# Kernel tuning notes

Hardware: AMD Instinct MI355X
Metric: run time of the kernel (lower is better)

The kernel has to match this reference:

```python
import jax, jax.numpy as jnp
import numpy as np

# module hyperparams (from init_kwargs)
C, O, G, E, W, KS = 64, 64, 16, 128, 7, 2
AH, AS = 2, 2              # activate_height, activate_stride
D = C // G                 # kernel depth per group = 4
N = O // G                 # filters per group = 4
EPS = 1e-5                 # BatchNorm eps
LEAKY = 0.01               # LeakyReLU negative slope
B, T = 2, 512


def setup_inputs() -> dict:
    key = jax.random.key(0)
    k1, k2 = jax.random.split(key)
    x = jax.random.normal(k1, (B, C, E, T), dtype=jnp.float32)
    weight = jax.random.normal(k2, (O, D, E, W), dtype=jnp.float32) * 0.05
    gamma = jnp.ones((O,), jnp.float32)
    beta = jnp.zeros((O,), jnp.float32)
    return {"x": x, "weight": weight, "gamma": gamma, "beta": beta}


def reference(x, weight, gamma, beta):
    b, c, f, T_in = x.shape
    pad = W // 2
    xp = jnp.pad(x, ((0, 0), (0, 0), (0, 0), (pad, pad)))
    t = (T_in + 2 * pad - W) // KS + 1
    # unfold: window index grid [t, W]
    idx = KS * jnp.arange(t)[:, None] + jnp.arange(W)[None, :]
    xu = xp[..., idx]                        # [b, c, f, t, W]
    xu = xu.reshape(b, G, D, f, t, W)        # channel = (g d), group-major
    wg = weight.reshape(G, N, D, f, W)       # out = (g n)
    # broadcast elementwise mul -> [b, g, n, d, f, t, w]
    y = xu[:, :, None] * wg[None, :, :, :, :, None, :]
    y = y.reshape(b, O, D, f, t, W)          # (g n) -> o
    # BatchNorm3d over channel O, training-mode batch stats (biased var)
    mean = y.mean(axis=(0, 2, 3, 4, 5), keepdims=True)
    var = y.var(axis=(0, 2, 3, 4, 5), keepdims=True)
    y = (y - mean) * jax.lax.rsqrt(var + EPS)
    bshape = (1, O, 1, 1, 1, 1)
    y = y * gamma.reshape(bshape) + beta.reshape(bshape)
    ys = y.sum(axis=(2, 5))                  # [b, o, f, t]
    yp = jax.lax.reduce_window(ys, jnp.float32(0), jax.lax.add,
                               (1, 1, AH, 1), (1, 1, AS, 1), 'VALID')  # [b,o,fo,t]
    return jnp.where(yp >= 0, yp, LEAKY * yp)
```

## Files before the change

### kernel.cpp

```cpp
#include <hip/hip_runtime.h>

constexpr int Cc = 64, Oc = 64, Gc = 16, Ec = 128, Wc = 7;
constexpr int Dc = 4, Nc = 4, Bc = 2, Tc = 512, TTc = 256, FOc = 64;
constexpr float EPSf = 1e-5f, LEAKYf = 0.01f;
constexpr float Minv = 1.0f / 1835008.0f;


__global__ __launch_bounds__(256) void stats_k(const float* __restrict__ x,
                                               const float* __restrict__ wgt,
                                               float* __restrict__ acc) {
  int bid = blockIdx.x;
  int fo  = bid & 63;
  int g   = (bid >> 6) & 15;
  int b   = bid >> 10;
  int tid = threadIdx.x;
  int d    = tid >> 6;
  int lane = tid & 63;

  __shared__ float part[4][4][2];

  float m_tot = 0.f, v_tot = 0.f;
#pragma unroll
  for (int f2 = 0; f2 < 2; ++f2) {
    int f = 2 * fo + f2;
    const float4* row4 =
        (const float4*)(x + ((size_t)((b * Cc + g * Dc + d) * Ec + f)) * Tc);
    float4 v0 = row4[lane];
    float4 v1 = row4[lane + 64];
    float se  = v0.x + v0.z + v1.x + v1.z;
    float so  = v0.y + v0.w + v1.y + v1.w;
    float se2 = v0.x * v0.x + v0.z * v0.z + v1.x * v1.x + v1.z * v1.z;
    float so2 = v0.y * v0.y + v0.w * v0.w + v1.y * v1.y + v1.w * v1.w;
#pragma unroll
    for (int off = 1; off < 64; off <<= 1) {
      se  += __shfl_xor(se, off);
      so  += __shfl_xor(so, off);
      se2 += __shfl_xor(se2, off);
      so2 += __shfl_xor(so2, off);
    }
    float x0   = __shfl(v0.x, 0);
    float x1   = __shfl(v0.y, 0);
    float x509 = __shfl(v1.y, 63);
    float x510 = __shfl(v1.z, 63);
    float x511 = __shfl(v1.w, 63);
    if (lane < 4) {
      float ws0 = so - x509 - x511, ws1 = se - x510, ws2 = so - x511;
      float ws3 = se, ws4 = so, ws5 = se - x0, ws6 = so - x1;
      float q0 = so2 - x509 * x509 - x511 * x511, q1 = se2 - x510 * x510;
      float q2 = so2 - x511 * x511, q3 = se2, q4 = so2;
      float q5 = se2 - x0 * x0, q6 = so2 - x1 * x1;
      int o = g * Nc + lane;
      const float* wp = wgt + ((size_t)((o * Dc + d) * Ec + f)) * Wc;
      float w0 = wp[0], w1 = wp[1], w2 = wp[2], w3 = wp[3], w4 = wp[4],
            w5 = wp[5], w6 = wp[6];
      m_tot += ws0 * w0 + ws1 * w1 + ws2 * w2 + ws3 * w3 + ws4 * w4 +
               ws5 * w5 + ws6 * w6;
      v_tot += q0 * w0 * w0 + q1 * w1 * w1 + q2 * w2 * w2 + q3 * w3 * w3 +
               q4 * w4 * w4 + q5 * w5 * w5 + q6 * w6 * w6;
    }
  }
  if (lane < 4) {
    part[d][lane][0] = m_tot;
    part[d][lane][1] = v_tot;
  }
  __syncthreads();
  if (tid < 8) {
    int n = tid >> 1, which = tid & 1;
    float tot = part[0][n][which] + part[1][n][which] + part[2][n][which] +
                part[3][n][which];
    int o = g * Nc + n;
    int slot = bid & 7;
    atomicAdd(&acc[(slot * 2 + which) * 64 + o], tot);
  }
}

__global__ __launch_bounds__(256) void conv_k(const float* __restrict__ x,
                                              const float* __restrict__ wgt,
                                              const float* __restrict__ gamma,
                                              const float* __restrict__ beta,
                                              const float* __restrict__ acc,
                                              float* __restrict__ out) {
  int bid = blockIdx.x;
  int fo  = bid & 63;
  int g   = (bid >> 6) & 15;
  int b   = bid >> 10;
  int tid = threadIdx.x;

  __shared__ float xs[8 * 520];
  __shared__ float wsm[224];
  __shared__ float sA[4], sC[4];

  {
    int f2 = tid >> 7;
    int j  = tid & 127;
#pragma unroll
    for (int dd = 0; dd < 4; ++dd) {
      const float4* src = (const float4*)(
          x + ((size_t)((b * Cc + g * Dc + dd) * Ec + 2 * fo + f2)) * Tc);
      float4 v  = src[j];
      float* row = &xs[(dd * 2 + f2) * 520];
      int q0 = 4 + 4 * j;
      row[((q0 + 0) & 7) * 65 + ((q0 + 0) >> 3)] = v.x;
      row[((q0 + 1) & 7) * 65 + ((q0 + 1) >> 3)] = v.y;
      row[((q0 + 2) & 7) * 65 + ((q0 + 2) >> 3)] = v.z;
      row[((q0 + 3) & 7) * 65 + ((q0 + 3) >> 3)] = v.w;
    }
  }
  if (tid < 64) {
    int r = tid >> 3, jj = tid & 7;
    int q = (jj < 4) ? jj : (512 + jj);
    xs[r * 520 + (q & 7) * 65 + (q >> 3)] = 0.f;
  }
  if (tid < 224) {
    int n = tid / 56, rr = tid % 56;
    int dd = rr / 14, r2 = rr % 14;
    int f2 = r2 / 7, w = r2 % 7;
    int o = g * Nc + n;
    wsm[tid] = wgt[((size_t)((o * Dc + dd) * Ec + 2 * fo + f2)) * Wc + w];
  } else if (tid < 228) {
    int n = tid - 224;
    int o = g * Nc + n;
    float msum = 0.f, esum = 0.f;
#pragma unroll
    for (int s = 0; s < 8; ++s) {
      msum += acc[(s * 2 + 0) * 64 + o];
      esum += acc[(s * 2 + 1) * 64 + o];
    }
    float mean = msum * Minv;
    float e2   = esum * Minv;
    float var  = e2 - mean * mean;
    float a    = gamma[o] * rsqrtf(var + EPSf);
    sA[n] = a;
    sC[n] = 56.0f * (beta[o] - a * mean);
  }
  __syncthreads();

  int n = tid >> 6;
  int j = tid & 63;
  float a0 = 0.f, a1 = 0.f, a2 = 0.f, a3 = 0.f;
#pragma unroll
  for (int r = 0; r < 8; ++r) {
    const float* row = &xs[r * 520];
    float xv[13];
#pragma unroll
    for (int i = 0; i < 13; ++i) {
      int c = 1 + i;
      xv[i] = row[(c & 7) * 65 + (c >> 3) + j];
    }
    const float* wp = &wsm[(n * 8 + r) * 7];
#pragma unroll
    for (int w = 0; w < 7; ++w) {
      float wt = wp[w];
      a0 += xv[w]     * wt;
      a1 += xv[w + 2] * wt;
      a2 += xv[w + 4] * wt;
      a3 += xv[w + 6] * wt;
    }
  }
  float sa = sA[n], sc = sC[n];
  float4 res;
  float r0 = sa * a0 + sc; res.x = (r0 >= 0.f) ? r0 : LEAKYf * r0;
  float r1 = sa * a1 + sc; res.y = (r1 >= 0.f) ? r1 : LEAKYf * r1;
  float r2 = sa * a2 + sc; res.z = (r2 >= 0.f) ? r2 : LEAKYf * r2;
  float r3 = sa * a3 + sc; res.w = (r3 >= 0.f) ? r3 : LEAKYf * r3;
  int o = g * Nc + n;
  float* op = out + ((size_t)((b * Oc + o) * FOc + fo)) * TTc + 4 * j;
  *(float4*)op = res;
}

extern "C" void kernel_launch(void* const* d_in, const int* in_sizes, int n_in,
                              void* d_out, int out_size, void* d_ws, size_t ws_size,
                              hipStream_t stream) {
  (void)in_sizes; (void)n_in; (void)out_size; (void)ws_size;
  const float* x     = (const float*)d_in[0];
  const float* w     = (const float*)d_in[1];
  const float* gamma = (const float*)d_in[2];
  const float* beta  = (const float*)d_in[3];
  float* acc = (float*)d_ws;
  hipMemsetAsync(acc, 0, 1024 * sizeof(float), stream);
  stats_k<<<dim3(Bc * Gc * FOc), dim3(256), 0, stream>>>(x, w, acc);
  conv_k<<<dim3(Bc * Gc * FOc), dim3(256), 0, stream>>>(x, w, gamma, beta, acc,
                                                        (float*)d_out);
}
```

Before: 91.71 us.

## Fuse stats into conv kernel, write raw sums, apply BN+LeakyReLU in finish pass

Replaces the separate stats kernel and the memset with a single fused pass. That pass reads x once, computes the raw windowed conv sums and writes them to workspace. It also produces per-block mean partials from the conv output and variance partials from shared-memory row sums of squares, which removes atomics. A second kernel reduces the partials per channel and applies the affine normalization and LeakyReLU to the raw buffer. The trade is one read of x in place of two, at the cost of an extra write and read of the full output-sized intermediate (about 8 MB).

```diff
diff --git a/kernel.cpp b/kernel.cpp
--- a/kernel.cpp
+++ b/kernel.cpp
@@ -6,80 +6,10 @@
 constexpr float Minv = 1.0f / 1835008.0f;
 
 
-__global__ __launch_bounds__(256) void stats_k(const float* __restrict__ x,
+__global__ __launch_bounds__(256) void fused_k(const float* __restrict__ x,
                                                const float* __restrict__ wgt,
-                                               float* __restrict__ acc) {
-  int bid = blockIdx.x;
-  int fo  = bid & 63;
-  int g   = (bid >> 6) & 15;
-  int b   = bid >> 10;
-  int tid = threadIdx.x;
-  int d    = tid >> 6;
-  int lane = tid & 63;
-
-  __shared__ float part[4][4][2];
-
-  float m_tot = 0.f, v_tot = 0.f;
-#pragma unroll
-  for (int f2 = 0; f2 < 2; ++f2) {
-    int f = 2 * fo + f2;
-    const float4* row4 =
-        (const float4*)(x + ((size_t)((b * Cc + g * Dc + d) * Ec + f)) * Tc);
-    float4 v0 = row4[lane];
-    float4 v1 = row4[lane + 64];
-    float se  = v0.x + v0.z + v1.x + v1.z;
-    float so  = v0.y + v0.w + v1.y + v1.w;
-    float se2 = v0.x * v0.x + v0.z * v0.z + v1.x * v1.x + v1.z * v1.z;
-    float so2 = v0.y * v0.y + v0.w * v0.w + v1.y * v1.y + v1.w * v1.w;
-#pragma unroll
-    for (int off = 1; off < 64; off <<= 1) {
-      se  += __shfl_xor(se, off);
-      so  += __shfl_xor(so, off);
-      se2 += __shfl_xor(se2, off);
-      so2 += __shfl_xor(so2, off);
-    }
-    float x0   = __shfl(v0.x, 0);
-    float x1   = __shfl(v0.y, 0);
-    float x509 = __shfl(v1.y, 63);
-    float x510 = __shfl(v1.z, 63);
-    float x511 = __shfl(v1.w, 63);
-    if (lane < 4) {
-      float ws0 = so - x509 - x511, ws1 = se - x510, ws2 = so - x511;
-      float ws3 = se, ws4 = so, ws5 = se - x0, ws6 = so - x1;
-      float q0 = so2 - x509 * x509 - x511 * x511, q1 = se2 - x510 * x510;
-      float q2 = so2 - x511 * x511, q3 = se2, q4 = so2;
-      float q5 = se2 - x0 * x0, q6 = so2 - x1 * x1;
-      int o = g * Nc + lane;
-      const float* wp = wgt + ((size_t)((o * Dc + d) * Ec + f)) * Wc;
-      float w0 = wp[0], w1 = wp[1], w2 = wp[2], w3 = wp[3], w4 = wp[4],
-            w5 = wp[5], w6 = wp[6];
-      m_tot += ws0 * w0 + ws1 * w1 + ws2 * w2 + ws3 * w3 + ws4 * w4 +
-               ws5 * w5 + ws6 * w6;
-      v_tot += q0 * w0 * w0 + q1 * w1 * w1 + q2 * w2 * w2 + q3 * w3 * w3 +
-               q4 * w4 * w4 + q5 * w5 * w5 + q6 * w6 * w6;
-    }
-  }
-  if (lane < 4) {
-    part[d][lane][0] = m_tot;
-    part[d][lane][1] = v_tot;
-  }
-  __syncthreads();
-  if (tid < 8) {
-    int n = tid >> 1, which = tid & 1;
-    float tot = part[0][n][which] + part[1][n][which] + part[2][n][which] +
-                part[3][n][which];
-    int o = g * Nc + n;
-    int slot = bid & 7;
-    atomicAdd(&acc[(slot * 2 + which) * 64 + o], tot);
-  }
-}
-
-__global__ __launch_bounds__(256) void conv_k(const float* __restrict__ x,
-                                              const float* __restrict__ wgt,
-                                              const float* __restrict__ gamma,
-                                              const float* __restrict__ beta,
-                                              const float* __restrict__ acc,
-                                              float* __restrict__ out) {
+                                               float* __restrict__ raw,
+                                               float* __restrict__ partials) {
   int bid = blockIdx.x;
   int fo  = bid & 63;
   int g   = (bid >> 6) & 15;
@@ -88,23 +18,25 @@
 
   __shared__ float xs[8 * 520];
   __shared__ float wsm[224];
-  __shared__ float sA[4], sC[4];
+  __shared__ float rowsum[4][4][2];
+  __shared__ float QL[8][7];
 
-  {
-    int f2 = tid >> 7;
-    int j  = tid & 127;
+  int f2 = tid >> 7;
+  int j  = tid & 127;
+  float se2p[4], so2p[4];
 #pragma unroll
-    for (int dd = 0; dd < 4; ++dd) {
-      const float4* src = (const float4*)(
-          x + ((size_t)((b * Cc + g * Dc + dd) * Ec + 2 * fo + f2)) * Tc);
-      float4 v  = src[j];
-      float* row = &xs[(dd * 2 + f2) * 520];
-      int q0 = 4 + 4 * j;
-      row[((q0 + 0) & 7) * 65 + ((q0 + 0) >> 3)] = v.x;
-      row[((q0 + 1) & 7) * 65 + ((q0 + 1) >> 3)] = v.y;
-      row[((q0 + 2) & 7) * 65 + ((q0 + 2) >> 3)] = v.z;
-      row[((q0 + 3) & 7) * 65 + ((q0 + 3) >> 3)] = v.w;
-    }
+  for (int dd = 0; dd < 4; ++dd) {
+    const float4* src = (const float4*)(
+        x + ((size_t)((b * Cc + g * Dc + dd) * Ec + 2 * fo + f2)) * Tc);
+    float4 v = src[j];
+    float* row = &xs[(dd * 2 + f2) * 520];
+    int q0 = 4 + 4 * j;
+    row[((q0 + 0) & 7) * 65 + ((q0 + 0) >> 3)] = v.x;
+    row[((q0 + 1) & 7) * 65 + ((q0 + 1) >> 3)] = v.y;
+    row[((q0 + 2) & 7) * 65 + ((q0 + 2) >> 3)] = v.z;
+    row[((q0 + 3) & 7) * 65 + ((q0 + 3) >> 3)] = v.w;
+    se2p[dd] = v.x * v.x + v.z * v.z;
+    so2p[dd] = v.y * v.y + v.w * v.w;
   }
   if (tid < 64) {
     int r = tid >> 3, jj = tid & 7;
@@ -114,29 +46,47 @@
   if (tid < 224) {
     int n = tid / 56, rr = tid % 56;
     int dd = rr / 14, r2 = rr % 14;
-    int f2 = r2 / 7, w = r2 % 7;
+    int ff = r2 / 7, w = r2 % 7;
     int o = g * Nc + n;
-    wsm[tid] = wgt[((size_t)((o * Dc + dd) * Ec + 2 * fo + f2)) * Wc + w];
-  } else if (tid < 228) {
-    int n = tid - 224;
-    int o = g * Nc + n;
-    float msum = 0.f, esum = 0.f;
+    wsm[tid] = wgt[((size_t)((o * Dc + dd) * Ec + 2 * fo + ff)) * Wc + w];
+  }
 #pragma unroll
-    for (int s = 0; s < 8; ++s) {
-      msum += acc[(s * 2 + 0) * 64 + o];
-      esum += acc[(s * 2 + 1) * 64 + o];
+  for (int off = 1; off < 64; off <<= 1) {
+#pragma unroll
+    for (int dd = 0; dd < 4; ++dd) {
+      se2p[dd] += __shfl_xor(se2p[dd], off);
+      so2p[dd] += __shfl_xor(so2p[dd], off);
     }
-    float mean = msum * Minv;
-    float e2   = esum * Minv;
-    float var  = e2 - mean * mean;
-    float a    = gamma[o] * rsqrtf(var + EPSf);
-    sA[n] = a;
-    sC[n] = 56.0f * (beta[o] - a * mean);
+  }
+  int lane = tid & 63, wv = tid >> 6;
+  if (lane == 0) {
+#pragma unroll
+    for (int dd = 0; dd < 4; ++dd) {
+      rowsum[wv][dd][0] = se2p[dd];
+      rowsum[wv][dd][1] = so2p[dd];
+    }
   }
   __syncthreads();
 
-  int n = tid >> 6;
-  int j = tid & 63;
+  if (tid < 8) {
+    int r = tid, ddi = r >> 1, f2i = r & 1;
+    const float* row = &xs[r * 520];
+    float e0 = row[260], e1 = row[325], e509 = row[129], e510 = row[194],
+          e511 = row[259];
+    float se2 = rowsum[f2i * 2][ddi][0] + rowsum[f2i * 2 + 1][ddi][0];
+    float so2 = rowsum[f2i * 2][ddi][1] + rowsum[f2i * 2 + 1][ddi][1];
+    QL[r][0] = so2 - e509 * e509 - e511 * e511;
+    QL[r][1] = se2 - e510 * e510;
+    QL[r][2] = so2 - e511 * e511;
+    QL[r][3] = se2;
+    QL[r][4] = so2;
+    QL[r][5] = se2 - e0 * e0;
+    QL[r][6] = so2 - e1 * e1;
+  }
+  __syncthreads();
+
+  int n  = tid >> 6;
+  int jj = tid & 63;
   float a0 = 0.f, a1 = 0.f, a2 = 0.f, a3 = 0.f;
 #pragma unroll
   for (int r = 0; r < 8; ++r) {
@@ -145,7 +95,7 @@
 #pragma unroll
     for (int i = 0; i < 13; ++i) {
       int c = 1 + i;
-      xv[i] = row[(c & 7) * 65 + (c >> 3) + j];
+      xv[i] = row[(c & 7) * 65 + (c >> 3) + jj];
     }
     const float* wp = &wsm[(n * 8 + r) * 7];
 #pragma unroll
@@ -157,15 +107,78 @@
       a3 += xv[w + 6] * wt;
     }
   }
-  float sa = sA[n], sc = sC[n];
+  int o = g * Nc + n;
+  float4 res; res.x = a0; res.y = a1; res.z = a2; res.w = a3;
+  *(float4*)(raw + ((size_t)((b * Oc + o) * FOc + fo)) * TTc + 4 * jj) = res;
+
+  float msum = a0 + a1 + a2 + a3;
+#pragma unroll
+  for (int off = 1; off < 64; off <<= 1) msum += __shfl_xor(msum, off);
+  if (jj == 0) partials[bid * 8 + n] = msum;
+
+  if (tid < 4) {
+    float vp = 0.f;
+#pragma unroll
+    for (int r = 0; r < 8; ++r) {
+#pragma unroll
+      for (int w = 0; w < 7; ++w) {
+        float wt = wsm[(tid * 8 + r) * 7 + w];
+        vp += QL[r][w] * wt * wt;
+      }
+    }
+    partials[bid * 8 + 4 + tid] = vp;
+  }
+}
+
+__global__ __launch_bounds__(256) void finish_k(const float* __restrict__ raw,
+                                                const float* __restrict__ partials,
+                                                const float* __restrict__ gamma,
+                                                const float* __restrict__ beta,
+                                                float* __restrict__ out) {
+  int bid = blockIdx.x;
+  int seg = bid & 15;
+  int o   = (bid >> 4) & 63;
+  int b   = bid >> 10;
+  int tid = threadIdx.x;
+  int g = o >> 2, n = o & 3;
+
+  __shared__ float red[2][2];
+  __shared__ float sAC[2];
+
+  float mp = 0.f, vp = 0.f;
+  if (tid < 128) {
+    int b2 = tid >> 6, fo = tid & 63;
+    const float* p = &partials[(size_t)(((b2 << 4) | g) << 6 | fo) * 8];
+    mp = p[n];
+    vp = p[4 + n];
+  }
+#pragma unroll
+  for (int off = 1; off < 64; off <<= 1) {
+    mp += __shfl_xor(mp, off);
+    vp += __shfl_xor(vp, off);
+  }
+  int lane = tid & 63, wv = tid >> 6;
+  if (lane == 0 && wv < 2) { red[wv][0] = mp; red[wv][1] = vp; }
+  __syncthreads();
+  if (tid == 0) {
+    float mean = (red[0][0] + red[1][0]) * Minv;
+    float e2   = (red[0][1] + red[1][1]) * Minv;
+    float var  = e2 - mean * mean;
+    float a    = gamma[o] * rsqrtf(var + EPSf);
+    sAC[0] = a;
+    sAC[1] = 56.0f * (beta[o] - a * mean);
+  }
+  __syncthreads();
+
+  float a = sAC[0], c = sAC[1];
+  size_t base = ((size_t)(b * Oc + o)) * (FOc * TTc) + seg * 1024 + tid * 4;
+  float4 v = *(const float4*)(raw + base);
   float4 res;
-  float r0 = sa * a0 + sc; res.x = (r0 >= 0.f) ? r0 : LEAKYf * r0;
-  float r1 = sa * a1 + sc; res.y = (r1 >= 0.f) ? r1 : LEAKYf * r1;
-  float r2 = sa * a2 + sc; res.z = (r2 >= 0.f) ? r2 : LEAKYf * r2;
-  float r3 = sa * a3 + sc; res.w = (r3 >= 0.f) ? r3 : LEAKYf * r3;
-  int o = g * Nc + n;
-  float* op = out + ((size_t)((b * Oc + o) * FOc + fo)) * TTc + 4 * j;
-  *(float4*)op = res;
+  float r0 = a * v.x + c; res.x = (r0 >= 0.f) ? r0 : LEAKYf * r0;
+  float r1 = a * v.y + c; res.y = (r1 >= 0.f) ? r1 : LEAKYf * r1;
+  float r2 = a * v.z + c; res.z = (r2 >= 0.f) ? r2 : LEAKYf * r2;
+  float r3 = a * v.w + c; res.w = (r3 >= 0.f) ? r3 : LEAKYf * r3;
+  *(float4*)(out + base) = res;
 }
 
 extern "C" void kernel_launch(void* const* d_in, const int* in_sizes, int n_in,
@@ -176,9 +189,9 @@
   const float* w     = (const float*)d_in[1];
   const float* gamma = (const float*)d_in[2];
   const float* beta  = (const float*)d_in[3];
-  float* acc = (float*)d_ws;
-  hipMemsetAsync(acc, 0, 1024 * sizeof(float), stream);
-  stats_k<<<dim3(Bc * Gc * FOc), dim3(256), 0, stream>>>(x, w, acc);
-  conv_k<<<dim3(Bc * Gc * FOc), dim3(256), 0, stream>>>(x, w, gamma, beta, acc,
-                                                        (float*)d_out);
+  float* raw      = (float*)d_ws;
+  float* partials = raw + (size_t)Bc * Oc * FOc * TTc;
+  fused_k<<<dim3(Bc * Gc * FOc), dim3(256), 0, stream>>>(x, w, raw, partials);
+  finish_k<<<dim3(Bc * Oc * 16), dim3(256), 0, stream>>>(raw, partials, gamma,
+                                                         beta, (float*)d_out);
 }
```

Result: no change. 92.87 us (+1.3%).
